# Performance work log

Hardware: AMD Instinct MI355X
Metric: run time of the kernel (lower is better)

## Reference

```python
import jax, jax.numpy as jnp
import numpy as np

N_NODES = 50000
N_EDGES = 800000
H = 128
CHEM_DIM = 34   # 2 + 2*num_gdf
GEOM_DIM = 48   # 2*num_gdf + num_signatures
EPS = 1e-5


def _linear_params(key, d_in, d_out):
    kw, kb = jax.random.split(key)
    lim = 1.0 / np.sqrt(d_in)
    w = jax.random.uniform(kw, (d_in, d_out), jnp.float32, -lim, lim)
    b = jax.random.uniform(kb, (d_out,), jnp.float32, -lim, lim)
    return w, b


def setup_inputs() -> dict:
    key = jax.random.key(0)
    ks = jax.random.split(key, 16)
    inp = {
        'chem_feats': jax.random.normal(ks[0], (N_EDGES, CHEM_DIM), jnp.float32),
        'geom_feats': jax.random.normal(ks[1], (N_NODES, GEOM_DIM), jnp.float32),
        'nbr_vids': jax.random.randint(ks[2], (N_EDGES,), 0, N_NODES, jnp.int32),
    }
    # chem_mlp: Linear(34,128) -> BN(128) -> SiLU -> Linear(128,256) -> BN(256)
    inp['w_c1'], inp['b_c1'] = _linear_params(ks[3], CHEM_DIM, H)
    inp['g_c1'], inp['be_c1'] = jnp.ones((H,), jnp.float32), jnp.zeros((H,), jnp.float32)
    inp['w_c2'], inp['b_c2'] = _linear_params(ks[4], H, 2 * H)
    inp['g_c2'], inp['be_c2'] = jnp.ones((2 * H,), jnp.float32), jnp.zeros((2 * H,), jnp.float32)
    # geom_mlp: Linear(48,64) -> BN(64) -> SiLU -> Linear(64,64) -> BN(64)
    inp['w_g1'], inp['b_g1'] = _linear_params(ks[5], GEOM_DIM, H // 2)
    inp['g_g1'], inp['be_g1'] = jnp.ones((H // 2,), jnp.float32), jnp.zeros((H // 2,), jnp.float32)
    inp['w_g2'], inp['b_g2'] = _linear_params(ks[6], H // 2, H // 2)
    inp['g_g2'], inp['be_g2'] = jnp.ones((H // 2,), jnp.float32), jnp.zeros((H // 2,), jnp.float32)
    # feat_mlp: Linear(192,128) -> BN(128) -> SiLU -> Linear(128,128) -> BN(128)
    inp['w_f1'], inp['b_f1'] = _linear_params(ks[7], H + H // 2, H)
    inp['g_f1'], inp['be_f1'] = jnp.ones((H,), jnp.float32), jnp.zeros((H,), jnp.float32)
    inp['w_f2'], inp['b_f2'] = _linear_params(ks[8], H, H)
    inp['g_f2'], inp['be_f2'] = jnp.ones((H,), jnp.float32), jnp.zeros((H,), jnp.float32)
    return inp


def _bn(x, gamma, beta):
    # BatchNorm1d with batch statistics (training-mode normalization; dropout = identity at eval)
    m = jnp.mean(x, axis=0)
    v = jnp.var(x, axis=0)
    return gamma * (x - m) * jax.lax.rsqrt(v + EPS) + beta


def reference(chem_feats, geom_feats, nbr_vids,
              w_c1, b_c1, g_c1, be_c1, w_c2, b_c2, g_c2, be_c2,
              w_g1, b_g1, g_g1, be_g1, w_g2, b_g2, g_g2, be_g2,
              w_f1, b_f1, g_f1, be_f1, w_f2, b_f2, g_f2, be_f2):
    # chem branch: per-edge MLP
    h = _bn(chem_feats @ w_c1 + b_c1, g_c1, be_c1)
    h = jax.nn.silu(h)
    h = _bn(h @ w_c2 + b_c2, g_c2, be_c2)            # [E, 2H]
    nbr_filter, nbr_core = jnp.split(h, 2, axis=-1)
    h_chem = jax.nn.sigmoid(nbr_filter) * jax.nn.softplus(nbr_core)  # [E, H]
    # scatter-sum per-edge features into node bins
    h_chem = jax.ops.segment_sum(h_chem, nbr_vids, num_segments=N_NODES)  # [N, H]
    # geom branch: per-node MLP
    hg = _bn(geom_feats @ w_g1 + b_g1, g_g1, be_g1)
    hg = jax.nn.silu(hg)
    h_geom = _bn(hg @ w_g2 + b_g2, g_g2, be_g2)      # [N, H/2]
    # fuse
    hf = jnp.concatenate((h_chem, h_geom), axis=-1)  # [N, 3H/2]
    hf = _bn(hf @ w_f1 + b_f1, g_f1, be_f1)
    hf = jax.nn.silu(hf)
    h_out = _bn(hf @ w_f2 + b_f2, g_f2, be_f2)       # [N, H]
    return h_out
```

## Files before the change

### kernel.cpp

```cpp
#include <hip/hip_runtime.h>
#include <hip/hip_bf16.h>
#include <cmath>

#define E_EDGES 800000
#define N_NODES 50000
#define BN_EPS 1e-5f

typedef __attribute__((ext_vector_type(8))) short short8;
typedef __attribute__((ext_vector_type(4))) float float4v;
typedef unsigned short ushort_t;

#define MFMA16(a, b, c) __builtin_amdgcn_mfma_f32_16x16x32_bf16((a), (b), (c), 0, 0, 0)

#define OFF_GX 0
#define OFF_GH 2304
#define OFF_A1 23040
#define OFF_C1 23168
#define OFF_A2 23296
#define OFF_C2 23552
#define OFF_GS1SUM 23808
#define OFF_GS1SQ 23872
#define OFF_GS2SUM 23936
#define OFF_GS2SQ 24000
#define OFF_FS1SUM 24064
#define OFF_FS1SQ 24192
#define OFF_FS2SUM 24320
#define OFF_FS2SQ 24448
#define OFF_NODE 24576
#define OFF_TG2 (OFF_NODE + N_NODES * 128)
#define OFF_TF1 (OFF_TG2 + N_NODES * 64)
#define OFF_TF2 OFF_NODE
#define OFF_W1T (OFF_TF1 + N_NODES * 128)
#define OFF_W2T (OFF_W1T + 4096)
#define OFF_BASEI (OFF_W2T + 16384)
#define OFF_BTOT (OFF_BASEI + 50176)
#define OFF_CNT (OFF_BTOT + 256)
#define OFF_CUR (OFF_CNT + 50176)
#define OFF_SIDX (OFF_CUR + 50176)
#define OFF_VIDS (OFF_SIDX + E_EDGES)

__device__ __forceinline__ float frcp_(float x) { return __builtin_amdgcn_rcpf(x); }
__device__ __forceinline__ float sigmoid_(float x) { return frcp_(1.0f + __expf(-x)); }
__device__ __forceinline__ float softplus_(float x) {
  return (x > 20.0f) ? x : __logf(1.0f + __expf(x));
}
__device__ __forceinline__ float silu_(float x) { return x * frcp_(1.0f + __expf(-x)); }

__device__ __forceinline__ ushort_t f2bf(float f) {
  __hip_bfloat16 h = __float2bfloat16(f);
  return *(ushort_t*)&h;
}
__device__ __forceinline__ float bf2f(ushort_t u) {
  return __uint_as_float(((unsigned)u) << 16);
}

__device__ __forceinline__ void load_xfrag(const float* __restrict__ chem, int e, int qd,
                                           short8* x0, short8* x1) {
  const float* xe = chem + e * 34;
  float2 p0 = *(const float2*)(xe + 8 * qd);
  float2 p1 = *(const float2*)(xe + 8 * qd + 2);
  float2 p2 = *(const float2*)(xe + 8 * qd + 4);
  float2 p3 = *(const float2*)(xe + 8 * qd + 6);
  short8 a;
  a[0] = (short)f2bf(p0.x); a[1] = (short)f2bf(p0.y);
  a[2] = (short)f2bf(p1.x); a[3] = (short)f2bf(p1.y);
  a[4] = (short)f2bf(p2.x); a[5] = (short)f2bf(p2.y);
  a[6] = (short)f2bf(p3.x); a[7] = (short)f2bf(p3.y);
  *x0 = a;
  short8 b = (short8){0, 0, 0, 0, 0, 0, 0, 0};
  if (qd == 0) {
    float2 pt = *(const float2*)(xe + 32);
    b[0] = (short)f2bf(pt.x); b[1] = (short)f2bf(pt.y);
  }
  *x1 = b;
}

__global__ __launch_bounds__(256) void k_prep(const float* __restrict__ w1,
                                              const float* __restrict__ w2,
                                              float* __restrict__ ws) {
  ushort_t* w1t = (ushort_t*)(ws + OFF_W1T);
  ushort_t* w2t = (ushort_t*)(ws + OFF_W2T);
  int idx = blockIdx.x * 256 + threadIdx.x;
  if (idx < 128 * 64) {
    int c = idx >> 6, k = idx & 63;
    float v = (k < 34) ? w1[k * 128 + c] : 0.0f;
    w1t[idx] = f2bf(v);
  }
  int j = idx - 128 * 64;
  if (j >= 0 && j < 256 * 128) {
    int c = j >> 7, k = j & 127;
    w2t[j] = f2bf(w2[k * 256 + c]);
  }
}

__global__ __launch_bounds__(256) void k_hist(const int* __restrict__ vids,
                                              float* __restrict__ ws) {
  const int e = blockIdx.x * 256 + threadIdx.x;
  int* cnt = (int*)(ws + OFF_CNT);
  if (e < E_EDGES) atomicAdd(&cnt[vids[e]], 1);
}

__global__ __launch_bounds__(256) void k_scan1(float* __restrict__ ws) {
  const int* cnt = (const int*)(ws + OFF_CNT);
  int* base = (int*)(ws + OFF_BASEI);
  int* btot = (int*)(ws + OFF_BTOT);
  const int t = threadIdx.x, b = blockIdx.x, i = b * 256 + t;
  const int lane = t & 63, w = t >> 6;
  int c = (i < N_NODES) ? cnt[i] : 0;
  int s = c;
#pragma unroll
  for (int o = 1; o < 64; o <<= 1) {
    int y = __shfl_up(s, o);
    if (lane >= o) s += y;
  }
  __shared__ int wsum[4];
  if (lane == 63) wsum[w] = s;
  __syncthreads();
  int add = 0;
#pragma unroll
  for (int k = 0; k < 4; ++k)
    if (k < w) add += wsum[k];
  base[i] = s + add - c;
  if (t == 255) btot[b] = s + add;
}

__global__ __launch_bounds__(256) void k_scan2(float* __restrict__ ws) {
  int* btot = (int*)(ws + OFF_BTOT);
  const int t = threadIdx.x;
  const int lane = t & 63, w = t >> 6;
  int c = (t < 196) ? btot[t] : 0;
  int s = c;
#pragma unroll
  for (int o = 1; o < 64; o <<= 1) {
    int y = __shfl_up(s, o);
    if (lane >= o) s += y;
  }
  __shared__ int wsum[4];
  if (lane == 63) wsum[w] = s;
  __syncthreads();
  int add = 0;
#pragma unroll
  for (int k = 0; k < 4; ++k)
    if (k < w) add += wsum[k];
  if (t < 196) btot[t] = s + add - c;
}

__global__ __launch_bounds__(256) void k_fill(const int* __restrict__ vids,
                                              float* __restrict__ ws) {
  const int e = blockIdx.x * 256 + threadIdx.x;
  const int* base = (const int*)(ws + OFF_BASEI);
  const int* btot = (const int*)(ws + OFF_BTOT);
  int* cur = (int*)(ws + OFF_CUR);
  int* sidx = (int*)(ws + OFF_SIDX);
  int* vsrt = (int*)(ws + OFF_VIDS);
  if (e < E_EDGES) {
    int v = vids[e];
    int pos = base[v] + btot[v >> 8] + atomicAdd(&cur[v], 1);
    sidx[pos] = e;
    vsrt[pos] = v;
  }
}

__global__ __launch_bounds__(256) void k_xstats(const float* __restrict__ chem,
                                                float* __restrict__ ws) {
  __shared__ __align__(16) ushort_t xT[2][48 * 72];
  const int t = threadIdx.x, wv = t >> 6, ln = t & 63, r15 = ln & 15, qd = ln >> 4;
  for (int i = t; i < 2 * 14 * 72; i += 256) {
    int b = i / (14 * 72), j = i % (14 * 72);
    int rr = j / 72, e = j % 72;
    xT[b][(34 + rr) * 72 + e] = (rr == 0 && e < 64) ? f2bf(1.0f) : (ushort_t)0;
  }
  float4v g0 = {0, 0, 0, 0}, g1 = {0, 0, 0, 0};
#pragma unroll 2
  for (int it = 0; it < 10; ++it) {
    const int st = blockIdx.x * 10 + it;
    const int buf = it & 1;
    for (int i = t; i < 64 * 34; i += 256) {
      int e = i / 34, k = i - e * 34;
      xT[buf][k * 72 + e] = f2bf(chem[st * 2176 + i]);
    }
    __syncthreads();
    const ushort_t* xb = &xT[buf][0];
#pragma unroll
    for (int ks = 0; ks < 2; ++ks) {
      const ushort_t* xk = xb + ks * 32 + 8 * qd;
      short8 f0 = *(const short8*)&xk[(0 + r15) * 72];
      short8 f1 = *(const short8*)&xk[(16 + r15) * 72];
      short8 f2v = *(const short8*)&xk[(32 + r15) * 72];
      if (wv == 0) { g0 = MFMA16(f0, f0, g0); g1 = MFMA16(f0, f1, g1); }
      else if (wv == 1) { g0 = MFMA16(f0, f2v, g0); g1 = MFMA16(f1, f1, g1); }
      else if (wv == 2) { g0 = MFMA16(f1, f2v, g0); }
      else { g0 = MFMA16(f2v, f2v, g0); }
    }
  }
  float* GX = ws + OFF_GX;
  int ti0, tj0, ti1 = -1, tj1 = -1;
  if (wv == 0) { ti0 = 0; tj0 = 0; ti1 = 0; tj1 = 1; }
  else if (wv == 1) { ti0 = 0; tj0 = 2; ti1 = 1; tj1 = 1; }
  else if (wv == 2) { ti0 = 1; tj0 = 2; }
  else { ti0 = 2; tj0 = 2; }
#pragma unroll
  for (int r = 0; r < 4; ++r)
    atomicAdd(&GX[(16 * ti0 + 4 * qd + r) * 48 + 16 * tj0 + r15], g0[r]);
  if (ti1 >= 0)
#pragma unroll
    for (int r = 0; r < 4; ++r)
      atomicAdd(&GX[(16 * ti1 + 4 * qd + r) * 48 + 16 * tj1 + r15], g1[r]);
}

__global__ __launch_bounds__(64) void k_bn1(const float* __restrict__ b1,
                                            const float* __restrict__ g1,
                                            const float* __restrict__ be1,
                                            float* __restrict__ ws) {
  const int c = blockIdx.x, i = threadIdx.x;
  __shared__ float wc[34];
  const ushort_t* w1t = (const ushort_t*)(ws + OFF_W1T);
  const float* GX = ws + OFF_GX;
  if (i < 34) wc[i] = bf2f(w1t[c * 64 + i]);
  __syncthreads();
  float p = 0.0f, ps = 0.0f;
  if (i < 34) {
    float gi = 0.0f;
    for (int j = 0; j < 34; ++j) {
      int a = i, b = j;
      if ((a >> 4) > (b >> 4)) { int tt = a; a = b; b = tt; }
      gi += GX[a * 48 + b] * wc[j];
    }
    p = wc[i] * gi;
    ps = wc[i] * GX[i * 48 + 34];
  }
#pragma unroll
  for (int off = 1; off < 64; off <<= 1) {
    p += __shfl_xor(p, off);
    ps += __shfl_xor(ps, off);
  }
  if (i == 0) {
    const float E = (float)E_EDGES;
    float bc = b1[c];
    float sum = ps + E * bc;
    float sq = p + 2.0f * bc * ps + E * bc * bc;
    float m = sum / E, v = sq / E - m * m;
    float a = g1[c] * rsqrtf(v + BN_EPS);
    ws[OFF_A1 + c] = a;
    ws[OFF_C1 + c] = a * (bc - m) + be1[c];
  }
}

template <int TJA, int TJB>
__device__ __forceinline__ void ghstep(const ushort_t* hk, int r15, float4v (&g)[11]) {
  short8 f[TJB + 1];
#pragma unroll
  for (int i = 0; i <= TJB; ++i) f[i] = *(const short8*)&hk[(16 * i + r15) * 72];
  short8 f8 = *(const short8*)&hk[(128 + r15) * 72];
  int s = 0;
#pragma unroll
  for (int ti = 0; ti <= TJA; ++ti) { g[s] = MFMA16(f[ti], f[TJA], g[s]); ++s; }
  g[s] = MFMA16(f8, f[TJA], g[s]); ++s;
#pragma unroll
  for (int ti = 0; ti <= TJB; ++ti) { g[s] = MFMA16(f[ti], f[TJB], g[s]); ++s; }
  g[s] = MFMA16(f8, f[TJB], g[s]);
}

__device__ __forceinline__ void ghtile(float* GH, int ti, int tj, int r15, int qd,
                                       const float4v v) {
#pragma unroll
  for (int r = 0; r < 4; ++r)
    atomicAdd(&GH[(16 * ti + 4 * qd + r) * 144 + 16 * tj + r15], v[r]);
}

template <int TJA, int TJB>
__device__ __forceinline__ void ghflush(float* GH, int r15, int qd, const float4v (&g)[11]) {
  int s = 0;
#pragma unroll
  for (int ti = 0; ti <= TJA; ++ti) { ghtile(GH, ti, TJA, r15, qd, g[s]); ++s; }
  ghtile(GH, 8, TJA, r15, qd, g[s]); ++s;
#pragma unroll
  for (int ti = 0; ti <= TJB; ++ti) { ghtile(GH, ti, TJB, r15, qd, g[s]); ++s; }
  ghtile(GH, 8, TJB, r15, qd, g[s]);
}

__global__ __launch_bounds__(256) void k_h(const float* __restrict__ chem,
                                           float* __restrict__ ws) {
  __shared__ __align__(16) ushort_t hT[2][144 * 72];
  const int t = threadIdx.x, wv = t >> 6, ln = t & 63, r15 = ln & 15, qd = ln >> 4;
  const ushort_t* w1t = (const ushort_t*)(ws + OFF_W1T);
  for (int i = t; i < 2 * 16 * 72; i += 256) {
    int b = i / (16 * 72), j = i % (16 * 72);
    int rr = j / 72, e = j % 72;
    hT[b][(128 + rr) * 72 + e] = (rr == 0 && e < 64) ? f2bf(1.0f) : (ushort_t)0;
  }
  float a1c[2], c1c[2];
#pragma unroll
  for (int cf = 0; cf < 2; ++cf) {
    int col = 32 * wv + 16 * cf + r15;
    a1c[cf] = ws[OFF_A1 + col];
    c1c[cf] = ws[OFF_C1 + col];
  }
  float4v gacc[11];
#pragma unroll
  for (int s = 0; s < 11; ++s) gacc[s] = (float4v){0, 0, 0, 0};

#pragma unroll 2
  for (int it = 0; it < 10; ++it) {
    const int st = blockIdx.x * 10 + it;
    const int buf = it & 1;
    const int e_base = st * 64;
    short8 xa0[4], xa1[4];
#pragma unroll
    for (int rb = 0; rb < 4; ++rb)
      load_xfrag(chem, e_base + 16 * rb + r15, qd, &xa0[rb], &xa1[rb]);
#pragma unroll
    for (int cf = 0; cf < 2; ++cf) {
      const int col = 32 * wv + 16 * cf + r15;
      short8 wb0 = *(const short8*)&w1t[col * 64 + 8 * qd];
      short8 wb1 = *(const short8*)&w1t[col * 64 + 32 + 8 * qd];
#pragma unroll
      for (int rb = 0; rb < 4; ++rb) {
        float4v acc = (float4v){0, 0, 0, 0};
        acc = MFMA16(xa0[rb], wb0, acc);
        acc = MFMA16(xa1[rb], wb1, acc);
        unsigned long long pk = 0;
#pragma unroll
        for (int r = 0; r < 4; ++r) {
          float hv = silu_(fmaf(a1c[cf], acc[r], c1c[cf]));
          pk |= ((unsigned long long)f2bf(hv)) << (16 * r);
        }
        *(unsigned long long*)&hT[buf][col * 72 + 16 * rb + 4 * qd] = pk;
      }
    }
    __syncthreads();
    const ushort_t* hb = &hT[buf][0];
#pragma unroll
    for (int ks = 0; ks < 2; ++ks) {
      const ushort_t* hk = hb + ks * 32 + 8 * qd;
      if (wv == 0) ghstep<0, 7>(hk, r15, gacc);
      else if (wv == 1) ghstep<1, 6>(hk, r15, gacc);
      else if (wv == 2) ghstep<2, 5>(hk, r15, gacc);
      else ghstep<3, 4>(hk, r15, gacc);
    }
  }
  float* GH = ws + OFF_GH;
  if (wv == 0) ghflush<0, 7>(GH, r15, qd, gacc);
  else if (wv == 1) ghflush<1, 6>(GH, r15, qd, gacc);
  else if (wv == 2) ghflush<2, 5>(GH, r15, qd, gacc);
  else ghflush<3, 4>(GH, r15, qd, gacc);
}

__global__ __launch_bounds__(128) void k_bn2(const float* __restrict__ b2,
                                             const float* __restrict__ g2,
                                             const float* __restrict__ be2,
                                             float* __restrict__ ws) {
  const int c = blockIdx.x, i = threadIdx.x;
  __shared__ float wcol[128];
  __shared__ float redQ[2], redS[2];
  const ushort_t* w2t = (const ushort_t*)(ws + OFF_W2T);
  const float* GH = ws + OFF_GH;
  wcol[i] = bf2f(w2t[c * 128 + i]);
  __syncthreads();
  float wi = wcol[i];
  float gi = 0.0f;
  for (int j = 0; j < 128; ++j) {
    int a = i, b = j;
    if ((a >> 4) > (b >> 4)) { int tt = a; a = b; b = tt; }
    gi += GH[a * 144 + b] * wcol[j];
  }
  float p = wi * gi;
  float ps = wi * GH[128 * 144 + i];
#pragma unroll
  for (int off = 1; off < 64; off <<= 1) {
    p += __shfl_xor(p, off);
    ps += __shfl_xor(ps, off);
  }
  const int wv = i >> 6, ln = i & 63;
  if (ln == 0) { redQ[wv] = p; redS[wv] = ps; }
  __syncthreads();
  if (i == 0) {
    float q = redQ[0] + redQ[1], s = redS[0] + redS[1];
    const float E = (float)E_EDGES;
    float bc = b2[c];
    float sum = s + E * bc;
    float sq = q + 2.0f * bc * s + E * bc * bc;
    float m = sum / E, v = sq / E - m * m;
    float a = g2[c] * rsqrtf(v + BN_EPS);
    ws[OFF_A2 + c] = a;
    ws[OFF_C2 + c] = a * (bc - m) + be2[c];
  }
}

__global__ __launch_bounds__(256) void k_scatter(const float* __restrict__ chem,
                                                 float* __restrict__ ws) {
  __shared__ __align__(16) ushort_t hS[64 * 136];
  __shared__ __align__(16) float gS[64 * 133];
  __shared__ int vS[64];
  const int t = threadIdx.x, wv = t >> 6, ln = t & 63, r15 = ln & 15, qd = ln >> 4;
  const ushort_t* w1t = (const ushort_t*)(ws + OFF_W1T);
  const ushort_t* w2t = (const ushort_t*)(ws + OFF_W2T);
  const int* sidx = (const int*)(ws + OFF_SIDX);
  const int* vsrt = (const int*)(ws + OFF_VIDS);
  float* node = ws + OFF_NODE;
  float a1c[2], c1c[2], aF2[2], cF2[2], aC2[2], cC2[2];
#pragma unroll
  for (int cf = 0; cf < 2; ++cf) {
    int col = 32 * wv + 16 * cf + r15;
    a1c[cf] = ws[OFF_A1 + col];
    c1c[cf] = ws[OFF_C1 + col];
    aF2[cf] = ws[OFF_A2 + col];
    cF2[cf] = ws[OFF_C2 + col];
    aC2[cf] = ws[OFF_A2 + 128 + col];
    cC2[cf] = ws[OFF_C2 + 128 + col];
  }
  for (int it = 0; it < 8; ++it) {
    const int st = blockIdx.x * 8 + it;
    if (st >= 12500) break;
    const int e_base = st * 64;
    const int myeid = sidx[e_base + ln];
    const int myvid = vsrt[e_base + ln];
    short8 xa0[4], xa1[4];
#pragma unroll
    for (int rb = 0; rb < 4; ++rb) {
      int er = __shfl(myeid, 16 * rb + r15);
      load_xfrag(chem, er, qd, &xa0[rb], &xa1[rb]);
    }
#pragma unroll
    for (int cf = 0; cf < 2; ++cf) {
      const int col = 32 * wv + 16 * cf + r15;
      short8 wb0 = *(const short8*)&w1t[col * 64 + 8 * qd];
      short8 wb1 = *(const short8*)&w1t[col * 64 + 32 + 8 * qd];
#pragma unroll
      for (int rb = 0; rb < 4; ++rb) {
        float4v acc = (float4v){0, 0, 0, 0};
        acc = MFMA16(xa0[rb], wb0, acc);
        acc = MFMA16(xa1[rb], wb1, acc);
#pragma unroll
        for (int r = 0; r < 4; ++r) {
          float hv = silu_(fmaf(a1c[cf], acc[r], c1c[cf]));
          hS[(16 * rb + 4 * qd + r) * 136 + col] = f2bf(hv);
        }
      }
    }
    __syncthreads();
    if (t < 64) vS[t] = myvid;
#pragma unroll
    for (int cf = 0; cf < 2; ++cf) {
      const int colF = 32 * wv + 16 * cf + r15;
      float4v accF[4], accC[4];
#pragma unroll
      for (int rb = 0; rb < 4; ++rb) {
        accF[rb] = (float4v){0, 0, 0, 0};
        accC[rb] = (float4v){0, 0, 0, 0};
      }
#pragma unroll
      for (int ks = 0; ks < 4; ++ks) {
        short8 bF = *(const short8*)&w2t[colF * 128 + ks * 32 + 8 * qd];
        short8 bC = *(const short8*)&w2t[(128 + colF) * 128 + ks * 32 + 8 * qd];
#pragma unroll
        for (int rb = 0; rb < 4; ++rb) {
          short8 hf = *(const short8*)&hS[(16 * rb + r15) * 136 + ks * 32 + 8 * qd];
          accF[rb] = MFMA16(hf, bF, accF[rb]);
          accC[rb] = MFMA16(hf, bC, accC[rb]);
        }
      }
#pragma unroll
      for (int rb = 0; rb < 4; ++rb)
#pragma unroll
        for (int r = 0; r < 4; ++r) {
          float F = fmaf(aF2[cf], accF[rb][r], cF2[cf]);
          float Co = fmaf(aC2[cf], accC[rb][r], cC2[cf]);
          gS[(16 * rb + 4 * qd + r) * 133 + colF] = sigmoid_(F) * softplus_(Co);
        }
    }
    __syncthreads();
    {
      const int c = t & 127, half = t >> 7;
      const float* g = &gS[(32 * half) * 133 + c];
      const int* vv = &vS[32 * half];
      float acc = g[0];
      int vcur = vv[0];
      for (int r = 1; r < 32; ++r) {
        int v = vv[r];
        float x = g[r * 133];
        if (v != vcur) {
          atomicAdd(node + (size_t)vcur * 128 + c, acc);
          acc = 0.0f;
          vcur = v;
        }
        acc += x;
      }
      atomicAdd(node + (size_t)vcur * 128 + c, acc);
    }
  }
}

__global__ __launch_bounds__(256) void k_geom_stats1(const float* __restrict__ geom,
                                                     const float* __restrict__ wg1,
                                                     const float* __restrict__ bg1,
                                                     float* __restrict__ ws) {
  __shared__ float ssum[64], ssq[64];
  const int t = threadIdx.x, lane = t & 63, w = t >> 6;
  if (t < 64) { ssum[t] = 0.0f; ssq[t] = 0.0f; }
  __syncthreads();
  const float bcol = bg1[lane];
  const int nb = blockIdx.x * 16 + w * 4;
  float x[4], acc[4];
#pragma unroll
  for (int u = 0; u < 4; u++) {
    x[u] = (lane < 48) ? geom[(nb + u) * 48 + lane] : 0.0f;
    acc[u] = bcol;
  }
#pragma unroll 16
  for (int k = 0; k < 48; k++) {
    float wvv = wg1[k * 64 + lane];
#pragma unroll
    for (int u = 0; u < 4; u++) acc[u] = fmaf(__shfl(x[u], k), wvv, acc[u]);
  }
  float bs = 0.0f, bq = 0.0f;
#pragma unroll
  for (int u = 0; u < 4; u++) { bs += acc[u]; bq += acc[u] * acc[u]; }
  atomicAdd(&ssum[lane], bs);
  atomicAdd(&ssq[lane], bq);
  __syncthreads();
  if (t < 64) {
    atomicAdd(ws + OFF_GS1SUM + t, ssum[t]);
    atomicAdd(ws + OFF_GS1SQ + t, ssq[t]);
  }
}

__global__ __launch_bounds__(256) void k_geom_main(
    const float* __restrict__ geom, const float* __restrict__ wg1,
    const float* __restrict__ bg1, const float* __restrict__ gg1,
    const float* __restrict__ beg1, const float* __restrict__ wg2,
    const float* __restrict__ bg2, float* __restrict__ ws) {
  __shared__ float ssum[64], ssq[64];
  const int t = threadIdx.x, lane = t & 63, w = t >> 6;
  if (t < 64) { ssum[t] = 0.0f; ssq[t] = 0.0f; }
  const float invN = 1.0f / (float)N_NODES;
  float s1 = ws[OFF_GS1SUM + lane], q1 = ws[OFF_GS1SQ + lane];
  float m1 = s1 * invN, v1 = q1 * invN - m1 * m1;
  float a1 = gg1[lane] * rsqrtf(v1 + BN_EPS);
  float c1 = beg1[lane] - a1 * m1;
  const float bcol = bg1[lane], b2col = bg2[lane];
  __syncthreads();
  const int nb = blockIdx.x * 16 + w * 4;
  float x[4], tg1[4], hg[4], acc[4];
#pragma unroll
  for (int u = 0; u < 4; u++) {
    x[u] = (lane < 48) ? geom[(nb + u) * 48 + lane] : 0.0f;
    tg1[u] = bcol;
  }
#pragma unroll 16
  for (int k = 0; k < 48; k++) {
    float wvv = wg1[k * 64 + lane];
#pragma unroll
    for (int u = 0; u < 4; u++) tg1[u] = fmaf(__shfl(x[u], k), wvv, tg1[u]);
  }
#pragma unroll
  for (int u = 0; u < 4; u++) {
    hg[u] = silu_(fmaf(a1, tg1[u], c1));
    acc[u] = b2col;
  }
#pragma unroll 16
  for (int k = 0; k < 64; k++) {
    float wvv = wg2[k * 64 + lane];
#pragma unroll
    for (int u = 0; u < 4; u++) acc[u] = fmaf(__shfl(hg[u], k), wvv, acc[u]);
  }
  float bs = 0.0f, bq = 0.0f;
#pragma unroll
  for (int u = 0; u < 4; u++) {
    ws[OFF_TG2 + (nb + u) * 64 + lane] = acc[u];
    bs += acc[u]; bq += acc[u] * acc[u];
  }
  atomicAdd(&ssum[lane], bs);
  atomicAdd(&ssq[lane], bq);
  __syncthreads();
  if (t < 64) {
    atomicAdd(ws + OFF_GS2SUM + t, ssum[t]);
    atomicAdd(ws + OFF_GS2SQ + t, ssq[t]);
  }
}

__global__ __launch_bounds__(256) void k_fuse1(const float* __restrict__ wf1,
                                               const float* __restrict__ bf1,
                                               const float* __restrict__ gg2,
                                               const float* __restrict__ beg2,
                                               float* __restrict__ ws) {
  __shared__ float ssum[128], ssq[128];
  const int t = threadIdx.x, lane = t & 63, w = t >> 6;
  if (t < 128) { ssum[t] = 0.0f; ssq[t] = 0.0f; }
  const float invN = 1.0f / (float)N_NODES;
  float s2 = ws[OFF_GS2SUM + lane], q2 = ws[OFF_GS2SQ + lane];
  float mg = s2 * invN, vg = q2 * invN - mg * mg;
  float ag = gg2[lane] * rsqrtf(vg + BN_EPS);
  float cg_ = beg2[lane] - ag * mg;
  const float bA = bf1[lane], bB = bf1[64 + lane];
  __syncthreads();
  const int nb = blockIdx.x * 16 + w * 4;
  float xa[4], xb[4], xg[4], acc1[4], acc2[4];
#pragma unroll
  for (int u = 0; u < 4; u++) {
    int n = nb + u;
    xa[u] = ws[OFF_NODE + n * 128 + lane];
    xb[u] = ws[OFF_NODE + n * 128 + 64 + lane];
    xg[u] = fmaf(ag, ws[OFF_TG2 + n * 64 + lane], cg_);
    acc1[u] = bA; acc2[u] = bB;
  }
#pragma unroll 16
  for (int k = 0; k < 64; k++) {
    float w1v = wf1[k * 128 + lane], w2v = wf1[k * 128 + 64 + lane];
#pragma unroll
    for (int u = 0; u < 4; u++) {
      float xk = __shfl(xa[u], k);
      acc1[u] = fmaf(xk, w1v, acc1[u]);
      acc2[u] = fmaf(xk, w2v, acc2[u]);
    }
  }
#pragma unroll 16
  for (int k = 0; k < 64; k++) {
    float w1v = wf1[(64 + k) * 128 + lane], w2v = wf1[(64 + k) * 128 + 64 + lane];
#pragma unroll
    for (int u = 0; u < 4; u++) {
      float xk = __shfl(xb[u], k);
      acc1[u] = fmaf(xk, w1v, acc1[u]);
      acc2[u] = fmaf(xk, w2v, acc2[u]);
    }
  }
#pragma unroll 16
  for (int k = 0; k < 64; k++) {
    float w1v = wf1[(128 + k) * 128 + lane], w2v = wf1[(128 + k) * 128 + 64 + lane];
#pragma unroll
    for (int u = 0; u < 4; u++) {
      float xk = __shfl(xg[u], k);
      acc1[u] = fmaf(xk, w1v, acc1[u]);
      acc2[u] = fmaf(xk, w2v, acc2[u]);
    }
  }
  float sA = 0, qA = 0, sB = 0, qB = 0;
#pragma unroll
  for (int u = 0; u < 4; u++) {
    int n = nb + u;
    ws[OFF_TF1 + n * 128 + lane] = acc1[u];
    ws[OFF_TF1 + n * 128 + 64 + lane] = acc2[u];
    sA += acc1[u]; qA += acc1[u] * acc1[u];
    sB += acc2[u]; qB += acc2[u] * acc2[u];
  }
  atomicAdd(&ssum[lane], sA); atomicAdd(&ssq[lane], qA);
  atomicAdd(&ssum[64 + lane], sB); atomicAdd(&ssq[64 + lane], qB);
  __syncthreads();
  if (t < 128) {
    atomicAdd(ws + OFF_FS1SUM + t, ssum[t]);
    atomicAdd(ws + OFF_FS1SQ + t, ssq[t]);
  }
}

__global__ __launch_bounds__(256) void k_fuse2(const float* __restrict__ wf2,
                                               const float* __restrict__ bf2,
                                               const float* __restrict__ gf1,
                                               const float* __restrict__ bef1,
                                               float* __restrict__ ws) {
  __shared__ float ssum[128], ssq[128];
  const int t = threadIdx.x, lane = t & 63, w = t >> 6;
  if (t < 128) { ssum[t] = 0.0f; ssq[t] = 0.0f; }
  const float invN = 1.0f / (float)N_NODES;
  float sA_ = ws[OFF_FS1SUM + lane], qA_ = ws[OFF_FS1SQ + lane];
  float mA = sA_ * invN, vA = qA_ * invN - mA * mA;
  float aA = gf1[lane] * rsqrtf(vA + BN_EPS);
  float cA = bef1[lane] - aA * mA;
  float sB_ = ws[OFF_FS1SUM + 64 + lane], qB_ = ws[OFF_FS1SQ + 64 + lane];
  float mB = sB_ * invN, vB = qB_ * invN - mB * mB;
  float aB = gf1[64 + lane] * rsqrtf(vB + BN_EPS);
  float cB = bef1[64 + lane] - aB * mB;
  const float b1c = bf2[lane], b2c = bf2[64 + lane];
  __syncthreads();
  const int nb = blockIdx.x * 16 + w * 4;
  float ha[4], hb[4], acc1[4], acc2[4];
#pragma unroll
  for (int u = 0; u < 4; u++) {
    int n = nb + u;
    ha[u] = silu_(fmaf(aA, ws[OFF_TF1 + n * 128 + lane], cA));
    hb[u] = silu_(fmaf(aB, ws[OFF_TF1 + n * 128 + 64 + lane], cB));
    acc1[u] = b1c; acc2[u] = b2c;
  }
#pragma unroll 16
  for (int k = 0; k < 64; k++) {
    float w1v = wf2[k * 128 + lane], w2v = wf2[k * 128 + 64 + lane];
#pragma unroll
    for (int u = 0; u < 4; u++) {
      float xk = __shfl(ha[u], k);
      acc1[u] = fmaf(xk, w1v, acc1[u]);
      acc2[u] = fmaf(xk, w2v, acc2[u]);
    }
  }
#pragma unroll 16
  for (int k = 0; k < 64; k++) {
    float w1v = wf2[(64 + k) * 128 + lane], w2v = wf2[(64 + k) * 128 + 64 + lane];
#pragma unroll
    for (int u = 0; u < 4; u++) {
      float xk = __shfl(hb[u], k);
      acc1[u] = fmaf(xk, w1v, acc1[u]);
      acc2[u] = fmaf(xk, w2v, acc2[u]);
    }
  }
  float sA = 0, qA = 0, sB = 0, qB = 0;
#pragma unroll
  for (int u = 0; u < 4; u++) {
    int n = nb + u;
    ws[OFF_TF2 + n * 128 + lane] = acc1[u];
    ws[OFF_TF2 + n * 128 + 64 + lane] = acc2[u];
    sA += acc1[u]; qA += acc1[u] * acc1[u];
    sB += acc2[u]; qB += acc2[u] * acc2[u];
  }
  atomicAdd(&ssum[lane], sA); atomicAdd(&ssq[lane], qA);
  atomicAdd(&ssum[64 + lane], sB); atomicAdd(&ssq[64 + lane], qB);
  __syncthreads();
  if (t < 128) {
    atomicAdd(ws + OFF_FS2SUM + t, ssum[t]);
    atomicAdd(ws + OFF_FS2SQ + t, ssq[t]);
  }
}

__global__ __launch_bounds__(256) void k_final(const float* __restrict__ gf2,
                                               const float* __restrict__ bef2,
                                               const float* __restrict__ ws,
                                               float* __restrict__ out) {
  const int idx = blockIdx.x * 256 + threadIdx.x;
  const int base = idx * 4;
  if (base >= N_NODES * 128) return;
  const float invN = 1.0f / (float)N_NODES;
  const int c0 = base & 127;
  float4 v = *(const float4*)(ws + OFF_TF2 + base);
  float vv[4] = {v.x, v.y, v.z, v.w}, r[4];
#pragma unroll
  for (int j = 0; j < 4; j++) {
    int c = c0 + j;
    float s = ws[OFF_FS2SUM + c], q = ws[OFF_FS2SQ + c];
    float m = s * invN, var = q * invN - m * m;
    float a = gf2[c] * rsqrtf(var + BN_EPS);
    r[j] = fmaf(a, vv[j] - m, bef2[c]);
  }
  *(float4*)(out + base) = make_float4(r[0], r[1], r[2], r[3]);
}

extern "C" void kernel_launch(void* const* d_in, const int* in_sizes, int n_in,
                              void* d_out, int out_size, void* d_ws, size_t ws_size,
                              hipStream_t stream) {
  const float* chem = (const float*)d_in[0];
  const float* geom = (const float*)d_in[1];
  const int* vids = (const int*)d_in[2];
  const float* w_c1 = (const float*)d_in[3];  const float* b_c1 = (const float*)d_in[4];
  const float* g_c1 = (const float*)d_in[5];  const float* be_c1 = (const float*)d_in[6];
  const float* w_c2 = (const float*)d_in[7];  const float* b_c2 = (const float*)d_in[8];
  const float* g_c2 = (const float*)d_in[9];  const float* be_c2 = (const float*)d_in[10];
  const float* w_g1 = (const float*)d_in[11]; const float* b_g1 = (const float*)d_in[12];
  const float* g_g1 = (const float*)d_in[13]; const float* be_g1 = (const float*)d_in[14];
  const float* w_g2 = (const float*)d_in[15]; const float* b_g2 = (const float*)d_in[16];
  const float* g_g2 = (const float*)d_in[17]; const float* be_g2 = (const float*)d_in[18];
  const float* w_f1 = (const float*)d_in[19]; const float* b_f1 = (const float*)d_in[20];
  const float* g_f1 = (const float*)d_in[21]; const float* be_f1 = (const float*)d_in[22];
  const float* w_f2 = (const float*)d_in[23]; const float* b_f2 = (const float*)d_in[24];
  const float* g_f2 = (const float*)d_in[25]; const float* be_f2 = (const float*)d_in[26];
  float* ws = (float*)d_ws;
  float* out = (float*)d_out;

  hipMemsetAsync(d_ws, 0, (size_t)(OFF_NODE + N_NODES * 128) * sizeof(float), stream);
  hipMemsetAsync((void*)(ws + OFF_CNT), 0, (size_t)(2 * 50176) * sizeof(int), stream);

  k_prep<<<dim3(160), dim3(256), 0, stream>>>(w_c1, w_c2, ws);
  k_hist<<<dim3(3125), dim3(256), 0, stream>>>(vids, ws);
  k_scan1<<<dim3(196), dim3(256), 0, stream>>>(ws);
  k_scan2<<<dim3(1), dim3(256), 0, stream>>>(ws);
  k_fill<<<dim3(3125), dim3(256), 0, stream>>>(vids, ws);
  k_xstats<<<dim3(1250), dim3(256), 0, stream>>>(chem, ws);
  k_bn1<<<dim3(128), dim3(64), 0, stream>>>(b_c1, g_c1, be_c1, ws);
  k_h<<<dim3(1250), dim3(256), 0, stream>>>(chem, ws);
  k_bn2<<<dim3(256), dim3(128), 0, stream>>>(b_c2, g_c2, be_c2, ws);
  k_scatter<<<dim3(1563), dim3(256), 0, stream>>>(chem, ws);
  k_geom_stats1<<<dim3(3125), dim3(256), 0, stream>>>(geom, w_g1, b_g1, ws);
  k_geom_main<<<dim3(3125), dim3(256), 0, stream>>>(geom, w_g1, b_g1, g_g1, be_g1, w_g2, b_g2, ws);
  k_fuse1<<<dim3(3125), dim3(256), 0, stream>>>(w_f1, b_f1, g_g2, be_g2, ws);
  k_fuse2<<<dim3(3125), dim3(256), 0, stream>>>(w_f2, b_f2, g_f1, be_f1, ws);
  k_final<<<dim3(6250), dim3(256), 0, stream>>>(g_f2, be_f2, ws, out);
}
```

Before: 1.173 ms.

## Use packed bf16 conversion, prefetch sorted indices, and halve scatter LDS staging

Replaces per-element float-to-bf16 conversion with the v_cvt_pk_bf16_f32 instruction and vectorizes the chem transpose load into float2 pairs. In the scatter kernel it prefetches the next tile's sorted edge and vertex ids during the current tile. It also processes the second GEMM and segmented atomic reduction in two 32-row halves, so the gS staging buffer shrinks by half. The aim is fewer ALU ops for conversion, hidden index-load latency, and lower LDS use for better occupancy. The cost is extra barriers per tile and shorter reduction runs, which can mean more atomics.

```diff
diff --git a/kernel.cpp b/kernel.cpp
--- a/kernel.cpp
+++ b/kernel.cpp
@@ -8,6 +8,7 @@
 
 typedef __attribute__((ext_vector_type(8))) short short8;
 typedef __attribute__((ext_vector_type(4))) float float4v;
+typedef __attribute__((ext_vector_type(4))) unsigned int uint4v;
 typedef unsigned short ushort_t;
 
 #define MFMA16(a, b, c) __builtin_amdgcn_mfma_f32_16x16x32_bf16((a), (b), (c), 0, 0, 0)
@@ -53,6 +54,11 @@
 __device__ __forceinline__ float bf2f(ushort_t u) {
   return __uint_as_float(((unsigned)u) << 16);
 }
+__device__ __forceinline__ unsigned cvtpk(float lo, float hi) {
+  unsigned r;
+  asm("v_cvt_pk_bf16_f32 %0, %1, %2" : "=v"(r) : "v"(lo), "v"(hi));
+  return r;
+}
 
 __device__ __forceinline__ void load_xfrag(const float* __restrict__ chem, int e, int qd,
                                            short8* x0, short8* x1) {
@@ -61,18 +67,19 @@
   float2 p1 = *(const float2*)(xe + 8 * qd + 2);
   float2 p2 = *(const float2*)(xe + 8 * qd + 4);
   float2 p3 = *(const float2*)(xe + 8 * qd + 6);
-  short8 a;
-  a[0] = (short)f2bf(p0.x); a[1] = (short)f2bf(p0.y);
-  a[2] = (short)f2bf(p1.x); a[3] = (short)f2bf(p1.y);
-  a[4] = (short)f2bf(p2.x); a[5] = (short)f2bf(p2.y);
-  a[6] = (short)f2bf(p3.x); a[7] = (short)f2bf(p3.y);
-  *x0 = a;
-  short8 b = (short8){0, 0, 0, 0, 0, 0, 0, 0};
+  union { short8 s; uint4v u; } cv;
+  cv.u[0] = cvtpk(p0.x, p0.y);
+  cv.u[1] = cvtpk(p1.x, p1.y);
+  cv.u[2] = cvtpk(p2.x, p2.y);
+  cv.u[3] = cvtpk(p3.x, p3.y);
+  *x0 = cv.s;
+  union { short8 s; uint4v u; } cb;
+  cb.u = (uint4v){0, 0, 0, 0};
   if (qd == 0) {
     float2 pt = *(const float2*)(xe + 32);
-    b[0] = (short)f2bf(pt.x); b[1] = (short)f2bf(pt.y);
-  }
-  *x1 = b;
+    cb.u[0] = cvtpk(pt.x, pt.y);
+  }
+  *x1 = cb.s;
 }
 
 __global__ __launch_bounds__(256) void k_prep(const float* __restrict__ w1,
@@ -168,16 +175,19 @@
   for (int i = t; i < 2 * 14 * 72; i += 256) {
     int b = i / (14 * 72), j = i % (14 * 72);
     int rr = j / 72, e = j % 72;
-    xT[b][(34 + rr) * 72 + e] = (rr == 0 && e < 64) ? f2bf(1.0f) : (ushort_t)0;
+    xT[b][(34 + rr) * 72 + e] = (rr == 0 && e < 64) ? (ushort_t)0x3F80 : (ushort_t)0;
   }
   float4v g0 = {0, 0, 0, 0}, g1 = {0, 0, 0, 0};
 #pragma unroll 2
   for (int it = 0; it < 10; ++it) {
     const int st = blockIdx.x * 10 + it;
     const int buf = it & 1;
-    for (int i = t; i < 64 * 34; i += 256) {
-      int e = i / 34, k = i - e * 34;
-      xT[buf][k * 72 + e] = f2bf(chem[st * 2176 + i]);
+    for (int i = t; i < 64 * 17; i += 256) {
+      int e = i / 17, kp = i - e * 17;
+      float2 v = *(const float2*)(chem + st * 2176 + e * 34 + 2 * kp);
+      unsigned u = cvtpk(v.x, v.y);
+      xT[buf][(2 * kp) * 72 + e] = (ushort_t)u;
+      xT[buf][(2 * kp + 1) * 72 + e] = (ushort_t)(u >> 16);
     }
     __syncthreads();
     const ushort_t* xb = &xT[buf][0];
@@ -287,7 +297,7 @@
   for (int i = t; i < 2 * 16 * 72; i += 256) {
     int b = i / (16 * 72), j = i % (16 * 72);
     int rr = j / 72, e = j % 72;
-    hT[b][(128 + rr) * 72 + e] = (rr == 0 && e < 64) ? f2bf(1.0f) : (ushort_t)0;
+    hT[b][(128 + rr) * 72 + e] = (rr == 0 && e < 64) ? (ushort_t)0x3F80 : (ushort_t)0;
   }
   float a1c[2], c1c[2];
 #pragma unroll
@@ -319,12 +329,12 @@
         float4v acc = (float4v){0, 0, 0, 0};
         acc = MFMA16(xa0[rb], wb0, acc);
         acc = MFMA16(xa1[rb], wb1, acc);
-        unsigned long long pk = 0;
-#pragma unroll
-        for (int r = 0; r < 4; ++r) {
-          float hv = silu_(fmaf(a1c[cf], acc[r], c1c[cf]));
-          pk |= ((unsigned long long)f2bf(hv)) << (16 * r);
-        }
+        float h0 = silu_(fmaf(a1c[cf], acc[0], c1c[cf]));
+        float h1 = silu_(fmaf(a1c[cf], acc[1], c1c[cf]));
+        float h2 = silu_(fmaf(a1c[cf], acc[2], c1c[cf]));
+        float h3 = silu_(fmaf(a1c[cf], acc[3], c1c[cf]));
+        unsigned lo = cvtpk(h0, h1), hi = cvtpk(h2, h3);
+        unsigned long long pk = ((unsigned long long)hi << 32) | (unsigned long long)lo;
         *(unsigned long long*)&hT[buf][col * 72 + 16 * rb + 4 * qd] = pk;
       }
     }
@@ -390,7 +400,7 @@
 __global__ __launch_bounds__(256) void k_scatter(const float* __restrict__ chem,
                                                  float* __restrict__ ws) {
   __shared__ __align__(16) ushort_t hS[64 * 136];
-  __shared__ __align__(16) float gS[64 * 133];
+  __shared__ __align__(16) float gS[32 * 133];
   __shared__ int vS[64];
   const int t = threadIdx.x, wv = t >> 6, ln = t & 63, r15 = ln & 15, qd = ln >> 4;
   const ushort_t* w1t = (const ushort_t*)(ws + OFF_W1T);
@@ -409,16 +419,21 @@
     aC2[cf] = ws[OFF_A2 + 128 + col];
     cC2[cf] = ws[OFF_C2 + 128 + col];
   }
+  const int st0 = blockIdx.x * 8;
+  int eid_cur = 0, vid_cur = 0;
+  if (st0 < 12500) { eid_cur = sidx[st0 * 64 + ln]; vid_cur = vsrt[st0 * 64 + ln]; }
   for (int it = 0; it < 8; ++it) {
-    const int st = blockIdx.x * 8 + it;
+    const int st = st0 + it;
     if (st >= 12500) break;
-    const int e_base = st * 64;
-    const int myeid = sidx[e_base + ln];
-    const int myvid = vsrt[e_base + ln];
+    int eid_nxt = 0, vid_nxt = 0;
+    if (it < 7 && st + 1 < 12500) {
+      eid_nxt = sidx[(st + 1) * 64 + ln];
+      vid_nxt = vsrt[(st + 1) * 64 + ln];
+    }
     short8 xa0[4], xa1[4];
 #pragma unroll
     for (int rb = 0; rb < 4; ++rb) {
-      int er = __shfl(myeid, 16 * rb + r15);
+      int er = __shfl(eid_cur, 16 * rb + r15);
       load_xfrag(chem, er, qd, &xa0[rb], &xa1[rb]);
     }
 #pragma unroll
@@ -434,60 +449,68 @@
 #pragma unroll
         for (int r = 0; r < 4; ++r) {
           float hv = silu_(fmaf(a1c[cf], acc[r], c1c[cf]));
-          hS[(16 * rb + 4 * qd + r) * 136 + col] = f2bf(hv);
+          hS[(16 * rb + 4 * qd + r) * 136 + col] = (ushort_t)cvtpk(hv, hv);
         }
       }
     }
     __syncthreads();
-    if (t < 64) vS[t] = myvid;
-#pragma unroll
-    for (int cf = 0; cf < 2; ++cf) {
-      const int colF = 32 * wv + 16 * cf + r15;
-      float4v accF[4], accC[4];
-#pragma unroll
-      for (int rb = 0; rb < 4; ++rb) {
-        accF[rb] = (float4v){0, 0, 0, 0};
-        accC[rb] = (float4v){0, 0, 0, 0};
+    if (t < 64) vS[t] = vid_cur;
+#pragma unroll
+    for (int ch = 0; ch < 2; ++ch) {
+#pragma unroll
+      for (int cf = 0; cf < 2; ++cf) {
+        const int colF = 32 * wv + 16 * cf + r15;
+        float4v accF[2], accC[2];
+#pragma unroll
+        for (int rbb = 0; rbb < 2; ++rbb) {
+          accF[rbb] = (float4v){0, 0, 0, 0};
+          accC[rbb] = (float4v){0, 0, 0, 0};
+        }
+#pragma unroll
+        for (int ks = 0; ks < 4; ++ks) {
+          short8 bF = *(const short8*)&w2t[colF * 128 + ks * 32 + 8 * qd];
+          short8 bC = *(const short8*)&w2t[(128 + colF) * 128 + ks * 32 + 8 * qd];
+#pragma unroll
+          for (int rbb = 0; rbb < 2; ++rbb) {
+            const int rb = 2 * ch + rbb;
+            short8 hf = *(const short8*)&hS[(16 * rb + r15) * 136 + ks * 32 + 8 * qd];
+            accF[rbb] = MFMA16(hf, bF, accF[rbb]);
+            accC[rbb] = MFMA16(hf, bC, accC[rbb]);
+          }
+        }
+#pragma unroll
+        for (int rbb = 0; rbb < 2; ++rbb)
+#pragma unroll
+          for (int r = 0; r < 4; ++r) {
+            float F = fmaf(aF2[cf], accF[rbb][r], cF2[cf]);
+            float Co = fmaf(aC2[cf], accC[rbb][r], cC2[cf]);
+            gS[(16 * rbb + 4 * qd + r) * 133 + colF] = sigmoid_(F) * softplus_(Co);
+          }
       }
-#pragma unroll
-      for (int ks = 0; ks < 4; ++ks) {
-        short8 bF = *(const short8*)&w2t[colF * 128 + ks * 32 + 8 * qd];
-        short8 bC = *(const short8*)&w2t[(128 + colF) * 128 + ks * 32 + 8 * qd];
-#pragma unroll
-        for (int rb = 0; rb < 4; ++rb) {
-          short8 hf = *(const short8*)&hS[(16 * rb + r15) * 136 + ks * 32 + 8 * qd];
-          accF[rb] = MFMA16(hf, bF, accF[rb]);
-          accC[rb] = MFMA16(hf, bC, accC[rb]);
+      __syncthreads();
+      {
+        const int c = t & 127, sub = t >> 7;
+        const float* g = &gS[(16 * sub) * 133 + c];
+        const int* vv = &vS[32 * ch + 16 * sub];
+        float acc = g[0];
+        int vcur = vv[0];
+#pragma unroll
+        for (int r = 1; r < 16; ++r) {
+          int v = vv[r];
+          float x = g[r * 133];
+          if (v != vcur) {
+            atomicAdd(node + (size_t)vcur * 128 + c, acc);
+            acc = 0.0f;
+            vcur = v;
+          }
+          acc += x;
         }
+        atomicAdd(node + (size_t)vcur * 128 + c, acc);
       }
-#pragma unroll
-      for (int rb = 0; rb < 4; ++rb)
-#pragma unroll
-        for (int r = 0; r < 4; ++r) {
-          float F = fmaf(aF2[cf], accF[rb][r], cF2[cf]);
-          float Co = fmaf(aC2[cf], accC[rb][r], cC2[cf]);
-          gS[(16 * rb + 4 * qd + r) * 133 + colF] = sigmoid_(F) * softplus_(Co);
-        }
-    }
-    __syncthreads();
-    {
-      const int c = t & 127, half = t >> 7;
-      const float* g = &gS[(32 * half) * 133 + c];
-      const int* vv = &vS[32 * half];
-      float acc = g[0];
-      int vcur = vv[0];
-      for (int r = 1; r < 32; ++r) {
-        int v = vv[r];
-        float x = g[r * 133];
-        if (v != vcur) {
-          atomicAdd(node + (size_t)vcur * 128 + c, acc);
-          acc = 0.0f;
-          vcur = v;
-        }
-        acc += x;
-      }
-      atomicAdd(node + (size_t)vcur * 128 + c, acc);
-    }
+      __syncthreads();
+    }
+    eid_cur = eid_nxt;
+    vid_cur = vid_nxt;
   }
 }
 
```

After: 1.283 ms. 9.4% more time.
